# Kernel optimization log

Measured on AMD Instinct MI355X. Metric: run time of the kernel, lower is better.

The kernel has to match this reference:

```python
import jax, jax.numpy as jnp
import numpy as np
import math

B, L, D = 4, 2048, 128
DEGREE = 2
EPS = 1e-12  # F.normalize eps

# upper-triangular index pairs (i <= j), matching torch.triu_indices(D, D)
_TRIU_I, _TRIU_J = np.triu_indices(D)
TRIU_I = jnp.asarray(_TRIU_I)
TRIU_J = jnp.asarray(_TRIU_J)


def setup_inputs() -> dict:
    key = jax.random.key(0)
    k1, _ = jax.random.split(key)
    x = jax.random.normal(k1, (B, L, D), dtype=jnp.float32)
    degree_scales = jnp.ones((DEGREE,), dtype=jnp.float32) / math.sqrt(DEGREE)
    return {"x": x, "degree_scales": degree_scales}


def reference(x, degree_scales):
    # F.normalize(x, dim=-1): x / max(||x||_2, eps)
    norm = jnp.linalg.norm(x, axis=-1, keepdims=True)
    x_norm = x / jnp.maximum(norm, EPS)
    # degree-1 features (unscaled, matching the torch code)
    feats1 = x_norm
    # degree-2 features: only the needed upper-triangular products, no D^2 materialization
    deg2 = x_norm[..., TRIU_I] * x_norm[..., TRIU_J]  # (B, L, D*(D+1)/2)
    deg2 = deg2 * degree_scales[1]
    return jnp.concatenate([feats1, deg2], axis=-1)  # (B, L, D + D*(D+1)/2)
```

## Files before the change

kernel.cpp:

```cpp
#include <hip/hip_runtime.h>


#define DD 128
#define ROW_OUT (DD + DD * (DD + 1) / 2)
#define NCHUNK (ROW_OUT / 4)

__global__ __launch_bounds__(256) void poly_kernel(
    const float* __restrict__ x, const float* __restrict__ scales,
    float* __restrict__ out) {
  __shared__ float s_img[ROW_OUT];

  const int row = blockIdx.x;
  const int tid = threadIdx.x;
  const float s1 = scales[1];

  if (tid < 64) {
    float4 xv = make_float4(0.f, 0.f, 0.f, 0.f);
    if (tid < 32) xv = ((const float4*)(x + (size_t)row * DD))[tid];
    float partial = xv.x * xv.x + xv.y * xv.y + xv.z * xv.z + xv.w * xv.w;
#pragma unroll
    for (int off = 16; off >= 1; off >>= 1)
      partial += __shfl_down(partial, off, 64);
    float total = __shfl(partial, 0, 64);
    float inv = 1.0f / fmaxf(sqrtf(total), 1e-12f);
    if (tid < 32)
      ((float4*)s_img)[tid] =
          make_float4(xv.x * inv, xv.y * inv, xv.z * inv, xv.w * inv);
  }
  __syncthreads();

  const int w = tid >> 6;
  const int lane = tid & 63;
  for (int i = w; i < DD; i += 4) {
    const float xi = s_img[i] * s1;
    const int len = DD - i;
    const int base = DD + ((i * (2 * DD + 1 - i)) >> 1);
    for (int l = lane; l < len; l += 64)
      s_img[base + l] = xi * s_img[i + l];
  }
  __syncthreads();

  float* orow = out + (size_t)row * ROW_OUT;
  for (int p4 = tid; p4 < NCHUNK; p4 += 256)
    ((float4*)orow)[p4] = ((const float4*)s_img)[p4];
}

extern "C" void kernel_launch(void* const* d_in, const int* in_sizes, int n_in,
                              void* d_out, int out_size, void* d_ws,
                              size_t ws_size, hipStream_t stream) {
  const float* x = (const float*)d_in[0];
  const float* scales = (const float*)d_in[1];
  float* out = (float*)d_out;
  const int n_rows = in_sizes[0] / DD;
  poly_kernel<<<n_rows, 256, 0, stream>>>(x, scales, out);
}
```

Measured before the change: 294.1 us.

## Write degree-2 products directly to global memory, skipping shared staging

```diff
diff --git a/kernel.cpp b/kernel.cpp
--- a/kernel.cpp
+++ b/kernel.cpp
@@ -3,46 +3,49 @@
 
 #define DD 128
 #define ROW_OUT (DD + DD * (DD + 1) / 2)
-#define NCHUNK (ROW_OUT / 4)
 
 __global__ __launch_bounds__(256) void poly_kernel(
     const float* __restrict__ x, const float* __restrict__ scales,
     float* __restrict__ out) {
-  __shared__ float s_img[ROW_OUT];
+  __shared__ float s_x[DD];
 
   const int row = blockIdx.x;
   const int tid = threadIdx.x;
-  const float s1 = scales[1];
+  const int w = tid >> 6;
+  const int lane = tid & 63;
 
-  if (tid < 64) {
-    float4 xv = make_float4(0.f, 0.f, 0.f, 0.f);
-    if (tid < 32) xv = ((const float4*)(x + (size_t)row * DD))[tid];
-    float partial = xv.x * xv.x + xv.y * xv.y + xv.z * xv.z + xv.w * xv.w;
+  const float* xr = x + (size_t)row * DD;
+  const float a = xr[lane];
+  const float b = xr[lane + 64];
+
+  if (w == 0) {
+    s_x[lane] = a;
+    s_x[lane + 64] = b;
+  }
+
+  float p = a * a + b * b;
 #pragma unroll
-    for (int off = 16; off >= 1; off >>= 1)
-      partial += __shfl_down(partial, off, 64);
-    float total = __shfl(partial, 0, 64);
-    float inv = 1.0f / fmaxf(sqrtf(total), 1e-12f);
-    if (tid < 32)
-      ((float4*)s_img)[tid] =
-          make_float4(xv.x * inv, xv.y * inv, xv.z * inv, xv.w * inv);
+  for (int off = 32; off >= 1; off >>= 1) p += __shfl_xor(p, off, 64);
+
+  const float c1 = 1.0f / fmaxf(sqrtf(p), 1e-12f);
+  const float c2 = c1 * c1 * scales[1];
+
+  float* orow = out + (size_t)row * ROW_OUT;
+  if (w == 1) {
+    orow[lane] = a * c1;
+    orow[lane + 64] = b * c1;
   }
   __syncthreads();
 
-  const int w = tid >> 6;
-  const int lane = tid & 63;
+#pragma unroll 4
   for (int i = w; i < DD; i += 4) {
-    const float xi = s_img[i] * s1;
+    const float xi = s_x[i] * c2;
     const int len = DD - i;
-    const int base = DD + ((i * (2 * DD + 1 - i)) >> 1);
-    for (int l = lane; l < len; l += 64)
-      s_img[base + l] = xi * s_img[i + l];
+    float* dst = orow + DD + ((i * (2 * DD + 1 - i)) >> 1);
+    if (lane < len) dst[lane] = xi * s_x[i + lane];
+    const int l2 = lane + 64;
+    if (l2 < len) dst[l2] = xi * s_x[i + l2];
   }
-  __syncthreads();
-
-  float* orow = out + (size_t)row * ROW_OUT;
-  for (int p4 = tid; p4 < NCHUNK; p4 += 256)
-    ((float4*)orow)[p4] = ((const float4*)s_img)[p4];
 }
 
 extern "C" void kernel_launch(void* const* d_in, const int* in_sizes, int n_in,
```

After: 282.8 us. -3.8%, faster.
